# Kernel tuning notes

Hardware: AMD Instinct MI355X
Metric: run time of the kernel (lower is better)

## Reference

```python
import jax, jax.numpy as jnp
import numpy as np

B, N, QD = 2, 4096, 512
HEADS, DIM_HEAD = 8, 64
INNER = HEADS * DIM_HEAD  # 512
SCALE = DIM_HEAD ** -0.5


def setup_inputs() -> dict:
    key = jax.random.key(0)
    ks = jax.random.split(key, 6)
    s = 0.02
    return {
        "x": jax.random.normal(ks[0], (B, N, QD), dtype=jnp.float32),
        "Wq": jax.random.normal(ks[1], (QD, INNER), dtype=jnp.float32) * s,
        "Wk": jax.random.normal(ks[2], (QD, INNER), dtype=jnp.float32) * s,
        "Wv": jax.random.normal(ks[3], (QD, INNER), dtype=jnp.float32) * s,
        "Wo": jax.random.normal(ks[4], (INNER, QD), dtype=jnp.float32) * s,
        "bo": jnp.zeros((QD,), dtype=jnp.float32),
    }


def reference(x, Wq, Wk, Wv, Wo, bo):
    # self-attention: context = x; mask = None; attention_sf = False
    q = x @ Wq  # [B, N, INNER]
    k = x @ Wk
    v = x @ Wv
    # split heads: [B, H, N, D]
    def split(t):
        return t.reshape(B, N, HEADS, DIM_HEAD).transpose(0, 2, 1, 3)
    q, k, v = split(q), split(k), split(v)
    # fp32 QK^T (ATTN_PRECISION='fp32' path)
    sim = jnp.einsum('bhid,bhjd->bhij', q.astype(jnp.float32), k.astype(jnp.float32)) * SCALE
    attn = jax.nn.softmax(sim, axis=-1)
    out = jnp.einsum('bhij,bhjd->bhid', attn, v)  # [B, H, N, D]
    out = out.transpose(0, 2, 1, 3).reshape(B, N, INNER)
    return out @ Wo + bo  # Dropout(p=0) is identity
```

## Files before the change

kernel.cpp:

```cpp
#include <hip/hip_runtime.h>
#include <hip/hip_bf16.h>


typedef __attribute__((ext_vector_type(8))) short short8;
typedef __attribute__((ext_vector_type(4))) float floatx4;

#define MFMA16(a, b, c) __builtin_amdgcn_mfma_f32_16x16x32_bf16((a), (b), (c), 0, 0, 0)

static __device__ __forceinline__ unsigned short f2b(float f) {
  unsigned int u = __float_as_uint(f);
  u += 0x7FFFu + ((u >> 16) & 1u);
  return (unsigned short)(u >> 16);
}

static __device__ __forceinline__ unsigned int pkb(float a, float b) {
  float2 t{a, b};
  __hip_bfloat162 h = __float22bfloat162_rn(t);
  union { __hip_bfloat162 h2; unsigned int u; } cv;
  cv.h2 = h;
  return cv.u;
}

__global__ __launch_bounds__(256) void wt_cvt_kernel(
    const float* __restrict__ Wq, const float* __restrict__ Wk,
    const float* __restrict__ Wv, const float* __restrict__ Wo,
    unsigned short* __restrict__ wtq, unsigned short* __restrict__ wtk,
    unsigned short* __restrict__ wtv, unsigned short* __restrict__ wto) {
  const int z = blockIdx.z;
  const float* __restrict__ W = (z == 0) ? Wq : (z == 1) ? Wk : (z == 2) ? Wv : Wo;
  unsigned short* __restrict__ T = (z == 0) ? wtq : (z == 1) ? wtk : (z == 2) ? wtv : wto;
  const int k0 = blockIdx.x * 32, c0 = blockIdx.y * 32;
  __shared__ float Ts[32][33];
  const int tid = threadIdx.x;
  const int r = tid >> 3, cc = (tid & 7) * 4;
  const float4 v = *(const float4*)(W + (k0 + r) * 512 + c0 + cc);
  Ts[r][cc] = v.x; Ts[r][cc + 1] = v.y; Ts[r][cc + 2] = v.z; Ts[r][cc + 3] = v.w;
  __syncthreads();
  const unsigned long long uu =
      (unsigned long long)pkb(Ts[cc][r], Ts[cc + 1][r]) |
      ((unsigned long long)pkb(Ts[cc + 2][r], Ts[cc + 3][r]) << 32);
  *(unsigned long long*)(T + (c0 + r) * 512 + k0 + cc) = uu;
}

__global__ __launch_bounds__(256) void qkv_proj_kernel(
    const float* __restrict__ x, const unsigned short* __restrict__ wtq,
    const unsigned short* __restrict__ wtk,
    const unsigned short* __restrict__ wtv, unsigned short* __restrict__ qo,
    unsigned short* __restrict__ ko, unsigned short* __restrict__ vo) {
  const int m0 = blockIdx.x * 64;
  const int c0 = blockIdx.y * 64;
  __shared__ __align__(16) unsigned short As[64 * 40];
  __shared__ __align__(16) unsigned short Bs[3][64 * 40];
  const int tid = threadIdx.x;
  const int lane = tid & 63, wvid = tid >> 6;
  const int i = lane & 15, q = lane >> 4;
  const int wy = wvid >> 1, wx = wvid & 1;
  const int arow = tid >> 2, acol = (tid & 3) * 8;
  floatx4 acc[3][2][2] = {};
  for (int k0 = 0; k0 < 512; k0 += 32) {
    __syncthreads();
    {
      const float* src = x + (m0 + arow) * 512 + k0 + acol;
      short8 av;
#pragma unroll
      for (int j = 0; j < 8; ++j) av[j] = (short)f2b(src[j]);
      *(short8*)&As[arow * 40 + acol] = av;
    }
    *(short8*)&Bs[0][arow * 40 + acol] =
        *(const short8*)(wtq + (c0 + arow) * 512 + k0 + acol);
    *(short8*)&Bs[1][arow * 40 + acol] =
        *(const short8*)(wtk + (c0 + arow) * 512 + k0 + acol);
    *(short8*)&Bs[2][arow * 40 + acol] =
        *(const short8*)(wtv + (c0 + arow) * 512 + k0 + acol);
    __syncthreads();
    short8 af[2];
#pragma unroll
    for (int t = 0; t < 2; ++t)
      af[t] = *(const short8*)&As[(wy * 32 + t * 16 + i) * 40 + q * 8];
#pragma unroll
    for (int z = 0; z < 3; ++z)
#pragma unroll
      for (int g = 0; g < 2; ++g) {
        const short8 bf =
            *(const short8*)&Bs[z][(wx * 32 + g * 16 + i) * 40 + q * 8];
#pragma unroll
        for (int t = 0; t < 2; ++t) acc[z][t][g] = MFMA16(af[t], bf, acc[z][t][g]);
      }
  }
#pragma unroll
  for (int z = 0; z < 3; ++z)
#pragma unroll
    for (int t = 0; t < 2; ++t)
#pragma unroll
      for (int g = 0; g < 2; ++g) {
        const int col = c0 + wx * 32 + g * 16 + i;
        const int h = col >> 6, d = col & 63;
        const int row0 = m0 + wy * 32 + t * 16 + q * 4;
        const int b = row0 >> 12;
        const int n0 = row0 & 4095;
        if (z == 2) {
          unsigned int* dst =
              (unsigned int*)&vo[(((b * 8 + h) * 64 + d) << 12) + n0];
          dst[0] = pkb(acc[z][t][g][0], acc[z][t][g][1]);
          dst[1] = pkb(acc[z][t][g][2], acc[z][t][g][3]);
        } else {
          unsigned short* dst = (z == 0) ? qo : ko;
          const float sc = (z == 0) ? 0.125f : 1.0f;
#pragma unroll
          for (int r = 0; r < 4; ++r)
            dst[(((b * 8 + h) << 12) + (n0 + r)) * 64 + d] =
                f2b(acc[z][t][g][r] * sc);
        }
      }
}

__global__ __launch_bounds__(256, 2) void flash_kernel(
    const unsigned short* __restrict__ Q, const unsigned short* __restrict__ K,
    const unsigned short* __restrict__ Vt, unsigned short* __restrict__ O) {
  const int bh = blockIdx.x;
  const int m0 = blockIdx.y * 128;
  const int tid = threadIdx.x;
  const int lane = tid & 63, w = tid >> 6;
  const int i = lane & 15, q = lane >> 4;
  const unsigned short* qp = Q + bh * (4096 * 64);
  const unsigned short* kp = K + bh * (4096 * 64);
  const unsigned short* vp = Vt + bh * (64 * 4096);

  __shared__ __align__(16) unsigned short Ks[2][64 * 72];
  __shared__ __align__(16) unsigned short Vs[2][64 * 72];
  __shared__ __align__(16) unsigned short Ps[4][32 * 72];

  const int srow = tid >> 3;
  const int scol = (tid & 7) * 8;
  const unsigned short* kg = kp + srow * 64 + scol;
  const unsigned short* vg = vp + srow * 4096 + scol;

  short8 qf[2][2];
#pragma unroll
  for (int t = 0; t < 2; ++t)
#pragma unroll
    for (int kc = 0; kc < 2; ++kc)
      qf[t][kc] = *(const short8*)(qp + (m0 + w * 32 + t * 16 + i) * 64 +
                                   kc * 32 + q * 8);

  floatx4 accO[2][4] = {};
  floatx4 accL[2] = {};
  short8 ones;
  {
    const short ov = (i == 0) ? (short)0x3F80 : (short)0;
#pragma unroll
    for (int j = 0; j < 8; ++j) ones[j] = ov;
  }
  const floatx4 zf = {0.f, 0.f, 0.f, 0.f};

  *(short8*)&Ks[0][srow * 72 + scol] = *(const short8*)(kg);
  *(short8*)&Ks[0][(srow + 32) * 72 + scol] = *(const short8*)(kg + 32 * 64);
  *(short8*)&Vs[0][srow * 72 + scol] = *(const short8*)(vg);
  *(short8*)&Vs[0][(srow + 32) * 72 + scol] = *(const short8*)(vg + 32 * 4096);
  __syncthreads();

  unsigned short* pw = &Ps[w][0];
  int cur = 0;
  for (int jt = 0; jt < 64; ++jt) {
    short8 kn0, kn1, vn0, vn1;
    if (jt < 63) {
      kn0 = *(const short8*)(kg + (jt + 1) * 4096);
      kn1 = *(const short8*)(kg + (jt + 1) * 4096 + 32 * 64);
      vn0 = *(const short8*)(vg + (jt + 1) * 64);
      vn1 = *(const short8*)(vg + (jt + 1) * 64 + 32 * 4096);
    }
    const unsigned short* Kc = &Ks[cur][0];
    const unsigned short* Vc = &Vs[cur][0];

#pragma unroll
    for (int g = 0; g < 4; ++g) {
      const short8 kf0 = *(const short8*)(Kc + (g * 16 + i) * 72 + q * 8);
      const short8 kf1 = *(const short8*)(Kc + (g * 16 + i) * 72 + 32 + q * 8);
#pragma unroll
      for (int t = 0; t < 2; ++t) {
        floatx4 s = MFMA16(kf0, qf[t][0], zf);
        s = MFMA16(kf1, qf[t][1], s);
        const float e0 = __expf(s[0]), e1 = __expf(s[1]);
        const float e2 = __expf(s[2]), e3 = __expf(s[3]);
        *(unsigned long long*)&pw[(t * 16 + i) * 72 + g * 16 + q * 4] =
            (unsigned long long)pkb(e0, e1) |
            ((unsigned long long)pkb(e2, e3) << 32);
      }
    }
    short8 pf[2][2];
#pragma unroll
    for (int t = 0; t < 2; ++t) {
      pf[t][0] = *(const short8*)(pw + (t * 16 + i) * 72 + q * 8);
      pf[t][1] = *(const short8*)(pw + (t * 16 + i) * 72 + 32 + q * 8);
      accL[t] = MFMA16(pf[t][0], ones, accL[t]);
      accL[t] = MFMA16(pf[t][1], ones, accL[t]);
    }
#pragma unroll
    for (int dg = 0; dg < 4; ++dg) {
      const short8 vf0 = *(const short8*)(Vc + (dg * 16 + i) * 72 + q * 8);
      const short8 vf1 = *(const short8*)(Vc + (dg * 16 + i) * 72 + 32 + q * 8);
#pragma unroll
      for (int t = 0; t < 2; ++t) {
        accO[t][dg] = MFMA16(pf[t][0], vf0, accO[t][dg]);
        accO[t][dg] = MFMA16(pf[t][1], vf1, accO[t][dg]);
      }
    }
    if (jt < 63) {
      *(short8*)&Ks[cur ^ 1][srow * 72 + scol] = kn0;
      *(short8*)&Ks[cur ^ 1][(srow + 32) * 72 + scol] = kn1;
      *(short8*)&Vs[cur ^ 1][srow * 72 + scol] = vn0;
      *(short8*)&Vs[cur ^ 1][(srow + 32) * 72 + scol] = vn1;
    }
    __syncthreads();
    cur ^= 1;
  }

  const int b = bh >> 3, h = bh & 7;
#pragma unroll
  for (int t = 0; t < 2; ++t) {
    float inv[4];
#pragma unroll
    for (int r = 0; r < 4; ++r) {
      const float l = __shfl(accL[t][r], lane & 48, 64);
      inv[r] = 1.0f / l;
    }
#pragma unroll
    for (int dg = 0; dg < 4; ++dg)
#pragma unroll
      for (int r = 0; r < 4; ++r) {
        const int n = m0 + w * 32 + t * 16 + q * 4 + r;
        const int col = h * 64 + dg * 16 + i;
        O[((b << 12) + n) * 512 + col] = f2b(accO[t][dg][r] * inv[r]);
      }
  }
}

__global__ __launch_bounds__(256) void out_proj_kernel(
    const unsigned short* __restrict__ A, const unsigned short* __restrict__ wto,
    const float* __restrict__ bo, float* __restrict__ out) {
  const int m0 = blockIdx.x * 64, c0 = blockIdx.y * 64;
  __shared__ __align__(16) unsigned short As[64 * 40];
  __shared__ __align__(16) unsigned short Bs[64 * 40];
  const int tid = threadIdx.x;
  const int lane = tid & 63, wvid = tid >> 6;
  const int i = lane & 15, q = lane >> 4;
  const int wy = wvid >> 1, wx = wvid & 1;
  const int arow = tid >> 2, acol = (tid & 3) * 8;
  floatx4 acc[2][2] = {};
  for (int k0 = 0; k0 < 512; k0 += 32) {
    __syncthreads();
    *(short8*)&As[arow * 40 + acol] =
        *(const short8*)(A + (m0 + arow) * 512 + k0 + acol);
    *(short8*)&Bs[arow * 40 + acol] =
        *(const short8*)(wto + (c0 + arow) * 512 + k0 + acol);
    __syncthreads();
    short8 af[2], bfr[2];
#pragma unroll
    for (int t = 0; t < 2; ++t)
      af[t] = *(const short8*)&As[(wy * 32 + t * 16 + i) * 40 + q * 8];
#pragma unroll
    for (int g = 0; g < 2; ++g)
      bfr[g] = *(const short8*)&Bs[(wx * 32 + g * 16 + i) * 40 + q * 8];
#pragma unroll
    for (int t = 0; t < 2; ++t)
#pragma unroll
      for (int g = 0; g < 2; ++g) acc[t][g] = MFMA16(af[t], bfr[g], acc[t][g]);
  }
#pragma unroll
  for (int t = 0; t < 2; ++t)
#pragma unroll
    for (int g = 0; g < 2; ++g) {
      const int col = c0 + wx * 32 + g * 16 + i;
      const float bias = bo[col];
#pragma unroll
      for (int r = 0; r < 4; ++r) {
        const int row = m0 + wy * 32 + t * 16 + q * 4 + r;
        out[row * 512 + col] = acc[t][g][r] + bias;
      }
    }
}

extern "C" void kernel_launch(void* const* d_in, const int* in_sizes, int n_in,
                              void* d_out, int out_size, void* d_ws,
                              size_t ws_size, hipStream_t stream) {
  const float* x = (const float*)d_in[0];
  const float* Wq = (const float*)d_in[1];
  const float* Wk = (const float*)d_in[2];
  const float* Wv = (const float*)d_in[3];
  const float* Wo = (const float*)d_in[4];
  const float* bo = (const float*)d_in[5];
  float* out = (float*)d_out;

  const size_t tsz = (size_t)16 * 4096 * 64;
  unsigned short* qws = (unsigned short*)d_ws;
  unsigned short* kws = qws + tsz;
  unsigned short* vws = kws + tsz;
  unsigned short* ows = vws + tsz;
  unsigned short* wtq = ows + tsz;
  unsigned short* wtk = wtq + 512 * 512;
  unsigned short* wtv = wtk + 512 * 512;
  unsigned short* wto = wtv + 512 * 512;

  wt_cvt_kernel<<<dim3(16, 16, 4), 256, 0, stream>>>(Wq, Wk, Wv, Wo, wtq, wtk,
                                                     wtv, wto);
  qkv_proj_kernel<<<dim3(128, 8), 256, 0, stream>>>(x, wtq, wtk, wtv, qws, kws,
                                                    vws);
  flash_kernel<<<dim3(16, 32), 256, 0, stream>>>(qws, kws, vws, ows);
  out_proj_kernel<<<dim3(128, 8), 256, 0, stream>>>(ows, wto, bo, out);
}
```

Before: 207.6 us.

## Enlarge GEMM tiles to 128x128, split QKV by grid z, single-buffer flash LDS

The QKV and output projection GEMMs move from 64x64 to 128x128 tiles with a 4x4 MFMA grid per wave. QKV now uses a separate grid z slice per weight matrix, so x is re-read and re-converted three times but each block reuses more data. The flash kernel drops K/V double buffering in shared memory, adds an extra barrier per iteration and raises launch_bounds min blocks to 4. The aim is higher occupancy in flash and better data reuse in the GEMMs, at the cost of serialising the LDS writes and fewer blocks in the projections.

```diff
diff --git a/kernel.cpp b/kernel.cpp
--- a/kernel.cpp
+++ b/kernel.cpp
@@ -47,74 +47,70 @@
     const unsigned short* __restrict__ wtk,
     const unsigned short* __restrict__ wtv, unsigned short* __restrict__ qo,
     unsigned short* __restrict__ ko, unsigned short* __restrict__ vo) {
-  const int m0 = blockIdx.x * 64;
-  const int c0 = blockIdx.y * 64;
-  __shared__ __align__(16) unsigned short As[64 * 40];
-  __shared__ __align__(16) unsigned short Bs[3][64 * 40];
+  const int z = blockIdx.z;
+  const unsigned short* __restrict__ wt = (z == 0) ? wtq : (z == 1) ? wtk : wtv;
+  const int m0 = blockIdx.x * 128;
+  const int c0 = blockIdx.y * 128;
+  __shared__ __align__(16) unsigned short As[128 * 40];
+  __shared__ __align__(16) unsigned short Bs[128 * 40];
   const int tid = threadIdx.x;
   const int lane = tid & 63, wvid = tid >> 6;
   const int i = lane & 15, q = lane >> 4;
   const int wy = wvid >> 1, wx = wvid & 1;
-  const int arow = tid >> 2, acol = (tid & 3) * 8;
-  floatx4 acc[3][2][2] = {};
+  const int arow = tid >> 1, ch = (tid & 1) * 16;
+  floatx4 acc[4][4] = {};
   for (int k0 = 0; k0 < 512; k0 += 32) {
     __syncthreads();
     {
-      const float* src = x + (m0 + arow) * 512 + k0 + acol;
-      short8 av;
-#pragma unroll
-      for (int j = 0; j < 8; ++j) av[j] = (short)f2b(src[j]);
-      *(short8*)&As[arow * 40 + acol] = av;
-    }
-    *(short8*)&Bs[0][arow * 40 + acol] =
-        *(const short8*)(wtq + (c0 + arow) * 512 + k0 + acol);
-    *(short8*)&Bs[1][arow * 40 + acol] =
-        *(const short8*)(wtk + (c0 + arow) * 512 + k0 + acol);
-    *(short8*)&Bs[2][arow * 40 + acol] =
-        *(const short8*)(wtv + (c0 + arow) * 512 + k0 + acol);
-    __syncthreads();
-    short8 af[2];
-#pragma unroll
-    for (int t = 0; t < 2; ++t)
-      af[t] = *(const short8*)&As[(wy * 32 + t * 16 + i) * 40 + q * 8];
-#pragma unroll
-    for (int z = 0; z < 3; ++z)
-#pragma unroll
-      for (int g = 0; g < 2; ++g) {
-        const short8 bf =
-            *(const short8*)&Bs[z][(wx * 32 + g * 16 + i) * 40 + q * 8];
-#pragma unroll
-        for (int t = 0; t < 2; ++t) acc[z][t][g] = MFMA16(af[t], bf, acc[z][t][g]);
-      }
-  }
-#pragma unroll
-  for (int z = 0; z < 3; ++z)
-#pragma unroll
-    for (int t = 0; t < 2; ++t)
-#pragma unroll
-      for (int g = 0; g < 2; ++g) {
-        const int col = c0 + wx * 32 + g * 16 + i;
-        const int h = col >> 6, d = col & 63;
-        const int row0 = m0 + wy * 32 + t * 16 + q * 4;
-        const int b = row0 >> 12;
-        const int n0 = row0 & 4095;
-        if (z == 2) {
-          unsigned int* dst =
-              (unsigned int*)&vo[(((b * 8 + h) * 64 + d) << 12) + n0];
-          dst[0] = pkb(acc[z][t][g][0], acc[z][t][g][1]);
-          dst[1] = pkb(acc[z][t][g][2], acc[z][t][g][3]);
-        } else {
-          unsigned short* dst = (z == 0) ? qo : ko;
-          const float sc = (z == 0) ? 0.125f : 1.0f;
-#pragma unroll
-          for (int r = 0; r < 4; ++r)
-            dst[(((b * 8 + h) << 12) + (n0 + r)) * 64 + d] =
-                f2b(acc[z][t][g][r] * sc);
-        }
-      }
-}
-
-__global__ __launch_bounds__(256, 2) void flash_kernel(
+      const float* src = x + (m0 + arow) * 512 + k0 + ch;
+      unsigned int av[8];
+#pragma unroll
+      for (int j = 0; j < 8; ++j) av[j] = pkb(src[2 * j], src[2 * j + 1]);
+      *(short8*)&As[arow * 40 + ch] = *(short8*)&av[0];
+      *(short8*)&As[arow * 40 + ch + 8] = *(short8*)&av[4];
+      const unsigned short* bs = wt + (c0 + arow) * 512 + k0 + ch;
+      *(short8*)&Bs[arow * 40 + ch] = *(const short8*)(bs);
+      *(short8*)&Bs[arow * 40 + ch + 8] = *(const short8*)(bs + 8);
+    }
+    __syncthreads();
+    short8 af[4], bfr[4];
+#pragma unroll
+    for (int t = 0; t < 4; ++t)
+      af[t] = *(const short8*)&As[(wy * 64 + t * 16 + i) * 40 + q * 8];
+#pragma unroll
+    for (int g = 0; g < 4; ++g)
+      bfr[g] = *(const short8*)&Bs[(wx * 64 + g * 16 + i) * 40 + q * 8];
+#pragma unroll
+    for (int t = 0; t < 4; ++t)
+#pragma unroll
+      for (int g = 0; g < 4; ++g) acc[t][g] = MFMA16(af[t], bfr[g], acc[t][g]);
+  }
+#pragma unroll
+  for (int t = 0; t < 4; ++t)
+#pragma unroll
+    for (int g = 0; g < 4; ++g) {
+      const int col = c0 + wx * 64 + g * 16 + i;
+      const int h = col >> 6, d = col & 63;
+      const int row0 = m0 + wy * 64 + t * 16 + q * 4;
+      const int b = row0 >> 12;
+      const int n0 = row0 & 4095;
+      if (z == 2) {
+        unsigned int* dst =
+            (unsigned int*)&vo[(((b * 8 + h) * 64 + d) << 12) + n0];
+        dst[0] = pkb(acc[t][g][0], acc[t][g][1]);
+        dst[1] = pkb(acc[t][g][2], acc[t][g][3]);
+      } else {
+        unsigned short* dst = (z == 0) ? qo : ko;
+        const float sc = (z == 0) ? 0.125f : 1.0f;
+#pragma unroll
+        for (int r = 0; r < 4; ++r)
+          dst[(((b * 8 + h) << 12) + (n0 + r)) * 64 + d] =
+              f2b(acc[t][g][r] * sc);
+      }
+    }
+}
+
+__global__ __launch_bounds__(256, 4) void flash_kernel(
     const unsigned short* __restrict__ Q, const unsigned short* __restrict__ K,
     const unsigned short* __restrict__ Vt, unsigned short* __restrict__ O) {
   const int bh = blockIdx.x;
@@ -126,8 +122,8 @@
   const unsigned short* kp = K + bh * (4096 * 64);
   const unsigned short* vp = Vt + bh * (64 * 4096);
 
-  __shared__ __align__(16) unsigned short Ks[2][64 * 72];
-  __shared__ __align__(16) unsigned short Vs[2][64 * 72];
+  __shared__ __align__(16) unsigned short Ks[64 * 72];
+  __shared__ __align__(16) unsigned short Vs[64 * 72];
   __shared__ __align__(16) unsigned short Ps[4][32 * 72];
 
   const int srow = tid >> 3;
@@ -153,14 +149,13 @@
   }
   const floatx4 zf = {0.f, 0.f, 0.f, 0.f};
 
-  *(short8*)&Ks[0][srow * 72 + scol] = *(const short8*)(kg);
-  *(short8*)&Ks[0][(srow + 32) * 72 + scol] = *(const short8*)(kg + 32 * 64);
-  *(short8*)&Vs[0][srow * 72 + scol] = *(const short8*)(vg);
-  *(short8*)&Vs[0][(srow + 32) * 72 + scol] = *(const short8*)(vg + 32 * 4096);
+  *(short8*)&Ks[srow * 72 + scol] = *(const short8*)(kg);
+  *(short8*)&Ks[(srow + 32) * 72 + scol] = *(const short8*)(kg + 32 * 64);
+  *(short8*)&Vs[srow * 72 + scol] = *(const short8*)(vg);
+  *(short8*)&Vs[(srow + 32) * 72 + scol] = *(const short8*)(vg + 32 * 4096);
   __syncthreads();
 
   unsigned short* pw = &Ps[w][0];
-  int cur = 0;
   for (int jt = 0; jt < 64; ++jt) {
     short8 kn0, kn1, vn0, vn1;
     if (jt < 63) {
@@ -169,13 +164,10 @@
       vn0 = *(const short8*)(vg + (jt + 1) * 64);
       vn1 = *(const short8*)(vg + (jt + 1) * 64 + 32 * 4096);
     }
-    const unsigned short* Kc = &Ks[cur][0];
-    const unsigned short* Vc = &Vs[cur][0];
-
 #pragma unroll
     for (int g = 0; g < 4; ++g) {
-      const short8 kf0 = *(const short8*)(Kc + (g * 16 + i) * 72 + q * 8);
-      const short8 kf1 = *(const short8*)(Kc + (g * 16 + i) * 72 + 32 + q * 8);
+      const short8 kf0 = *(const short8*)(&Ks[(g * 16 + i) * 72 + q * 8]);
+      const short8 kf1 = *(const short8*)(&Ks[(g * 16 + i) * 72 + 32 + q * 8]);
 #pragma unroll
       for (int t = 0; t < 2; ++t) {
         floatx4 s = MFMA16(kf0, qf[t][0], zf);
@@ -197,22 +189,22 @@
     }
 #pragma unroll
     for (int dg = 0; dg < 4; ++dg) {
-      const short8 vf0 = *(const short8*)(Vc + (dg * 16 + i) * 72 + q * 8);
-      const short8 vf1 = *(const short8*)(Vc + (dg * 16 + i) * 72 + 32 + q * 8);
+      const short8 vf0 = *(const short8*)(&Vs[(dg * 16 + i) * 72 + q * 8]);
+      const short8 vf1 = *(const short8*)(&Vs[(dg * 16 + i) * 72 + 32 + q * 8]);
 #pragma unroll
       for (int t = 0; t < 2; ++t) {
         accO[t][dg] = MFMA16(pf[t][0], vf0, accO[t][dg]);
         accO[t][dg] = MFMA16(pf[t][1], vf1, accO[t][dg]);
       }
     }
+    __syncthreads();
     if (jt < 63) {
-      *(short8*)&Ks[cur ^ 1][srow * 72 + scol] = kn0;
-      *(short8*)&Ks[cur ^ 1][(srow + 32) * 72 + scol] = kn1;
-      *(short8*)&Vs[cur ^ 1][srow * 72 + scol] = vn0;
-      *(short8*)&Vs[cur ^ 1][(srow + 32) * 72 + scol] = vn1;
-    }
-    __syncthreads();
-    cur ^= 1;
+      *(short8*)&Ks[srow * 72 + scol] = kn0;
+      *(short8*)&Ks[(srow + 32) * 72 + scol] = kn1;
+      *(short8*)&Vs[srow * 72 + scol] = vn0;
+      *(short8*)&Vs[(srow + 32) * 72 + scol] = vn1;
+    }
+    __syncthreads();
   }
 
   const int b = bh >> 3, h = bh & 7;
@@ -238,43 +230,47 @@
 __global__ __launch_bounds__(256) void out_proj_kernel(
     const unsigned short* __restrict__ A, const unsigned short* __restrict__ wto,
     const float* __restrict__ bo, float* __restrict__ out) {
-  const int m0 = blockIdx.x * 64, c0 = blockIdx.y * 64;
-  __shared__ __align__(16) unsigned short As[64 * 40];
-  __shared__ __align__(16) unsigned short Bs[64 * 40];
+  const int m0 = blockIdx.x * 128, c0 = blockIdx.y * 128;
+  __shared__ __align__(16) unsigned short As[128 * 40];
+  __shared__ __align__(16) unsigned short Bs[128 * 40];
   const int tid = threadIdx.x;
   const int lane = tid & 63, wvid = tid >> 6;
   const int i = lane & 15, q = lane >> 4;
   const int wy = wvid >> 1, wx = wvid & 1;
-  const int arow = tid >> 2, acol = (tid & 3) * 8;
-  floatx4 acc[2][2] = {};
+  const int arow = tid >> 1, ch = (tid & 1) * 16;
+  floatx4 acc[4][4] = {};
   for (int k0 = 0; k0 < 512; k0 += 32) {
     __syncthreads();
-    *(short8*)&As[arow * 40 + acol] =
-        *(const short8*)(A + (m0 + arow) * 512 + k0 + acol);
-    *(short8*)&Bs[arow * 40 + acol] =
-        *(const short8*)(wto + (c0 + arow) * 512 + k0 + acol);
-    __syncthreads();
-    short8 af[2], bfr[2];
-#pragma unroll
-    for (int t = 0; t < 2; ++t)
-      af[t] = *(const short8*)&As[(wy * 32 + t * 16 + i) * 40 + q * 8];
-#pragma unroll
-    for (int g = 0; g < 2; ++g)
-      bfr[g] = *(const short8*)&Bs[(wx * 32 + g * 16 + i) * 40 + q * 8];
-#pragma unroll
-    for (int t = 0; t < 2; ++t)
-#pragma unroll
-      for (int g = 0; g < 2; ++g) acc[t][g] = MFMA16(af[t], bfr[g], acc[t][g]);
-  }
-#pragma unroll
-  for (int t = 0; t < 2; ++t)
-#pragma unroll
-    for (int g = 0; g < 2; ++g) {
-      const int col = c0 + wx * 32 + g * 16 + i;
+    {
+      const unsigned short* as = A + (m0 + arow) * 512 + k0 + ch;
+      *(short8*)&As[arow * 40 + ch] = *(const short8*)(as);
+      *(short8*)&As[arow * 40 + ch + 8] = *(const short8*)(as + 8);
+      const unsigned short* bs = wto + (c0 + arow) * 512 + k0 + ch;
+      *(short8*)&Bs[arow * 40 + ch] = *(const short8*)(bs);
+      *(short8*)&Bs[arow * 40 + ch + 8] = *(const short8*)(bs + 8);
+    }
+    __syncthreads();
+    short8 af[4], bfr[4];
+#pragma unroll
+    for (int t = 0; t < 4; ++t)
+      af[t] = *(const short8*)&As[(wy * 64 + t * 16 + i) * 40 + q * 8];
+#pragma unroll
+    for (int g = 0; g < 4; ++g)
+      bfr[g] = *(const short8*)&Bs[(wx * 64 + g * 16 + i) * 40 + q * 8];
+#pragma unroll
+    for (int t = 0; t < 4; ++t)
+#pragma unroll
+      for (int g = 0; g < 4; ++g) acc[t][g] = MFMA16(af[t], bfr[g], acc[t][g]);
+  }
+#pragma unroll
+  for (int t = 0; t < 4; ++t)
+#pragma unroll
+    for (int g = 0; g < 4; ++g) {
+      const int col = c0 + wx * 64 + g * 16 + i;
       const float bias = bo[col];
 #pragma unroll
       for (int r = 0; r < 4; ++r) {
-        const int row = m0 + wy * 32 + t * 16 + q * 4 + r;
+        const int row = m0 + wy * 64 + t * 16 + q * 4 + r;
         out[row * 512 + col] = acc[t][g][r] + bias;
       }
     }
@@ -303,8 +299,8 @@
 
   wt_cvt_kernel<<<dim3(16, 16, 4), 256, 0, stream>>>(Wq, Wk, Wv, Wo, wtq, wtk,
                                                      wtv, wto);
-  qkv_proj_kernel<<<dim3(128, 8), 256, 0, stream>>>(x, wtq, wtk, wtv, qws, kws,
-                                                    vws);
+  qkv_proj_kernel<<<dim3(64, 4, 3), 256, 0, stream>>>(x, wtq, wtk, wtv, qws,
+                                                      kws, vws);
   flash_kernel<<<dim3(16, 32), 256, 0, stream>>>(qws, kws, vws, ows);
-  out_proj_kernel<<<dim3(128, 8), 256, 0, stream>>>(ows, wto, bo, out);
-}
+  out_proj_kernel<<<dim3(64, 4), 256, 0, stream>>>(ows, wto, bo, out);
+}
```

Result: slower. 225.5 us (+8.6%).

## Split flash attention KV range across two wave groups with swizzled LDS and exp2

Applied to the files above, without the earlier changes.

The flash kernel grows to 512 threads. Two groups of four waves each process half of the 4096 keys for the same 128 query rows, and their partial O and row sums are merged through shared memory at the end. The padded LDS layout is replaced by an XOR swizzle, and the old double buffer becomes a single buffer guarded by two barriers per step. The softmax scale is folded with log2(e) into Q so that a hardware exp2 can stand in for expf. Together these aim at more waves per CU and cheaper exponentials, at the cost of an extra barrier per step and a final reduction pass.

```diff
diff --git a/kernel.cpp b/kernel.cpp
--- a/kernel.cpp
+++ b/kernel.cpp
@@ -6,6 +6,14 @@
 typedef __attribute__((ext_vector_type(4))) float floatx4;
 
 #define MFMA16(a, b, c) __builtin_amdgcn_mfma_f32_16x16x32_bf16((a), (b), (c), 0, 0, 0)
+
+#if __has_builtin(__builtin_amdgcn_exp2f)
+#define EXP2(x) __builtin_amdgcn_exp2f(x)
+#else
+#define EXP2(x) exp2f(x)
+#endif
+
+#define QSCALE 0.18033688011112042f
 
 static __device__ __forceinline__ unsigned short f2b(float f) {
   unsigned int u = __float_as_uint(f);
@@ -105,7 +113,7 @@
           dst[1] = pkb(acc[z][t][g][2], acc[z][t][g][3]);
         } else {
           unsigned short* dst = (z == 0) ? qo : ko;
-          const float sc = (z == 0) ? 0.125f : 1.0f;
+          const float sc = (z == 0) ? QSCALE : 1.0f;
 #pragma unroll
           for (int r = 0; r < 4; ++r)
             dst[(((b * 8 + h) << 12) + (n0 + r)) * 64 + d] =
@@ -114,7 +122,7 @@
       }
 }
 
-__global__ __launch_bounds__(256, 2) void flash_kernel(
+__global__ __launch_bounds__(512, 4) void flash_kernel(
     const unsigned short* __restrict__ Q, const unsigned short* __restrict__ K,
     const unsigned short* __restrict__ Vt, unsigned short* __restrict__ O) {
   const int bh = blockIdx.x;
@@ -122,25 +130,29 @@
   const int tid = threadIdx.x;
   const int lane = tid & 63, w = tid >> 6;
   const int i = lane & 15, q = lane >> 4;
+  const int rt = w & 3;
+  const int kg = w >> 2;
   const unsigned short* qp = Q + bh * (4096 * 64);
   const unsigned short* kp = K + bh * (4096 * 64);
   const unsigned short* vp = Vt + bh * (64 * 4096);
 
-  __shared__ __align__(16) unsigned short Ks[2][64 * 72];
-  __shared__ __align__(16) unsigned short Vs[2][64 * 72];
-  __shared__ __align__(16) unsigned short Ps[4][32 * 72];
-
-  const int srow = tid >> 3;
-  const int scol = (tid & 7) * 8;
-  const unsigned short* kg = kp + srow * 64 + scol;
-  const unsigned short* vg = vp + srow * 4096 + scol;
+  __shared__ __align__(16) unsigned short SM[32768];
+  unsigned short* Ks = SM + kg * 4096;
+  unsigned short* Vs = SM + 8192 + kg * 4096;
+  unsigned short* pw = SM + 16384 + w * 2048;
+
+  const int srow = (tid & 255) >> 3;
+  const int c0s = tid & 7;
+  const int sw8 = (c0s ^ (srow & 7)) * 8;
+  const unsigned short* kgp = kp + (kg * 2048 + srow) * 64 + c0s * 8;
+  const unsigned short* vgp = vp + srow * 4096 + kg * 2048 + c0s * 8;
 
   short8 qf[2][2];
 #pragma unroll
   for (int t = 0; t < 2; ++t)
 #pragma unroll
     for (int kc = 0; kc < 2; ++kc)
-      qf[t][kc] = *(const short8*)(qp + (m0 + w * 32 + t * 16 + i) * 64 +
+      qf[t][kc] = *(const short8*)(qp + (m0 + rt * 32 + t * 16 + i) * 64 +
                                    kc * 32 + q * 8);
 
   floatx4 accO[2][4] = {};
@@ -153,36 +165,36 @@
   }
   const floatx4 zf = {0.f, 0.f, 0.f, 0.f};
 
-  *(short8*)&Ks[0][srow * 72 + scol] = *(const short8*)(kg);
-  *(short8*)&Ks[0][(srow + 32) * 72 + scol] = *(const short8*)(kg + 32 * 64);
-  *(short8*)&Vs[0][srow * 72 + scol] = *(const short8*)(vg);
-  *(short8*)&Vs[0][(srow + 32) * 72 + scol] = *(const short8*)(vg + 32 * 4096);
+  const int sl = i & 7;
+
+  *(short8*)&Ks[srow * 64 + sw8] = *(const short8*)(kgp);
+  *(short8*)&Ks[(srow + 32) * 64 + sw8] = *(const short8*)(kgp + 32 * 64);
+  *(short8*)&Vs[srow * 64 + sw8] = *(const short8*)(vgp);
+  *(short8*)&Vs[(srow + 32) * 64 + sw8] = *(const short8*)(vgp + 32 * 4096);
   __syncthreads();
 
-  unsigned short* pw = &Ps[w][0];
-  int cur = 0;
-  for (int jt = 0; jt < 64; ++jt) {
+  for (int jt = 0; jt < 32; ++jt) {
     short8 kn0, kn1, vn0, vn1;
-    if (jt < 63) {
-      kn0 = *(const short8*)(kg + (jt + 1) * 4096);
-      kn1 = *(const short8*)(kg + (jt + 1) * 4096 + 32 * 64);
-      vn0 = *(const short8*)(vg + (jt + 1) * 64);
-      vn1 = *(const short8*)(vg + (jt + 1) * 64 + 32 * 4096);
-    }
-    const unsigned short* Kc = &Ks[cur][0];
-    const unsigned short* Vc = &Vs[cur][0];
-
+    if (jt < 31) {
+      kn0 = *(const short8*)(kgp + (jt + 1) * 4096);
+      kn1 = *(const short8*)(kgp + (jt + 1) * 4096 + 32 * 64);
+      vn0 = *(const short8*)(vgp + (jt + 1) * 64);
+      vn1 = *(const short8*)(vgp + (jt + 1) * 64 + 32 * 4096);
+    }
 #pragma unroll
     for (int g = 0; g < 4; ++g) {
-      const short8 kf0 = *(const short8*)(Kc + (g * 16 + i) * 72 + q * 8);
-      const short8 kf1 = *(const short8*)(Kc + (g * 16 + i) * 72 + 32 + q * 8);
+      const short8 kf0 = *(const short8*)(&Ks[(g * 16 + i) * 64 + (q ^ sl) * 8]);
+      const short8 kf1 =
+          *(const short8*)(&Ks[(g * 16 + i) * 64 + ((4 + q) ^ sl) * 8]);
 #pragma unroll
       for (int t = 0; t < 2; ++t) {
         floatx4 s = MFMA16(kf0, qf[t][0], zf);
         s = MFMA16(kf1, qf[t][1], s);
-        const float e0 = __expf(s[0]), e1 = __expf(s[1]);
-        const float e2 = __expf(s[2]), e3 = __expf(s[3]);
-        *(unsigned long long*)&pw[(t * 16 + i) * 72 + g * 16 + q * 4] =
+        const float e0 = EXP2(s[0]), e1 = EXP2(s[1]);
+        const float e2 = EXP2(s[2]), e3 = EXP2(s[3]);
+        *(unsigned long long*)&pw[(t * 16 + i) * 64 +
+                                  (((2 * g + (q >> 1)) ^ sl) * 8) +
+                                  (q & 1) * 4] =
             (unsigned long long)pkb(e0, e1) |
             ((unsigned long long)pkb(e2, e3) << 32);
       }
@@ -190,29 +202,59 @@
     short8 pf[2][2];
 #pragma unroll
     for (int t = 0; t < 2; ++t) {
-      pf[t][0] = *(const short8*)(pw + (t * 16 + i) * 72 + q * 8);
-      pf[t][1] = *(const short8*)(pw + (t * 16 + i) * 72 + 32 + q * 8);
+      pf[t][0] = *(const short8*)(pw + (t * 16 + i) * 64 + (q ^ sl) * 8);
+      pf[t][1] = *(const short8*)(pw + (t * 16 + i) * 64 + ((4 + q) ^ sl) * 8);
       accL[t] = MFMA16(pf[t][0], ones, accL[t]);
       accL[t] = MFMA16(pf[t][1], ones, accL[t]);
     }
 #pragma unroll
     for (int dg = 0; dg < 4; ++dg) {
-      const short8 vf0 = *(const short8*)(Vc + (dg * 16 + i) * 72 + q * 8);
-      const short8 vf1 = *(const short8*)(Vc + (dg * 16 + i) * 72 + 32 + q * 8);
+      const short8 vf0 =
+          *(const short8*)(&Vs[(dg * 16 + i) * 64 + (q ^ sl) * 8]);
+      const short8 vf1 =
+          *(const short8*)(&Vs[(dg * 16 + i) * 64 + ((4 + q) ^ sl) * 8]);
 #pragma unroll
       for (int t = 0; t < 2; ++t) {
         accO[t][dg] = MFMA16(pf[t][0], vf0, accO[t][dg]);
         accO[t][dg] = MFMA16(pf[t][1], vf1, accO[t][dg]);
       }
     }
-    if (jt < 63) {
-      *(short8*)&Ks[cur ^ 1][srow * 72 + scol] = kn0;
-      *(short8*)&Ks[cur ^ 1][(srow + 32) * 72 + scol] = kn1;
-      *(short8*)&Vs[cur ^ 1][srow * 72 + scol] = vn0;
-      *(short8*)&Vs[cur ^ 1][(srow + 32) * 72 + scol] = vn1;
-    }
-    __syncthreads();
-    cur ^= 1;
+    __syncthreads();
+    if (jt < 31) {
+      *(short8*)&Ks[srow * 64 + sw8] = kn0;
+      *(short8*)&Ks[(srow + 32) * 64 + sw8] = kn1;
+      *(short8*)&Vs[srow * 64 + sw8] = vn0;
+      *(short8*)&Vs[(srow + 32) * 64 + sw8] = vn1;
+    }
+    __syncthreads();
+  }
+
+  float* MB = (float*)SM;
+  if (kg == 1) {
+    float* dst = MB + (rt * 64 + lane) * 40;
+#pragma unroll
+    for (int t = 0; t < 2; ++t) {
+#pragma unroll
+      for (int dg = 0; dg < 4; ++dg)
+#pragma unroll
+        for (int r = 0; r < 4; ++r) dst[t * 16 + dg * 4 + r] = accO[t][dg][r];
+#pragma unroll
+      for (int r = 0; r < 4; ++r) dst[32 + t * 4 + r] = accL[t][r];
+    }
+  }
+  __syncthreads();
+  if (kg == 1) return;
+  {
+    const float* src = MB + (rt * 64 + lane) * 40;
+#pragma unroll
+    for (int t = 0; t < 2; ++t) {
+#pragma unroll
+      for (int dg = 0; dg < 4; ++dg)
+#pragma unroll
+        for (int r = 0; r < 4; ++r) accO[t][dg][r] += src[t * 16 + dg * 4 + r];
+#pragma unroll
+      for (int r = 0; r < 4; ++r) accL[t][r] += src[32 + t * 4 + r];
+    }
   }
 
   const int b = bh >> 3, h = bh & 7;
@@ -228,7 +270,7 @@
     for (int dg = 0; dg < 4; ++dg)
 #pragma unroll
       for (int r = 0; r < 4; ++r) {
-        const int n = m0 + w * 32 + t * 16 + q * 4 + r;
+        const int n = m0 + rt * 32 + t * 16 + q * 4 + r;
         const int col = h * 64 + dg * 16 + i;
         O[((b << 12) + n) * 512 + col] = f2b(accO[t][dg][r] * inv[r]);
       }
@@ -305,6 +347,6 @@
                                                      wtv, wto);
   qkv_proj_kernel<<<dim3(128, 8), 256, 0, stream>>>(x, wtq, wtk, wtv, qws, kws,
                                                     vws);
-  flash_kernel<<<dim3(16, 32), 256, 0, stream>>>(qws, kws, vws, ows);
+  flash_kernel<<<dim3(16, 32), 512, 0, stream>>>(qws, kws, vws, ows);
   out_proj_kernel<<<dim3(128, 8), 256, 0, stream>>>(ows, wto, bo, out);
 }
```

After: 197.9 us. 1.05x faster.
